# Performance work log

Hardware: AMD Instinct MI355X
Metric: run time of the kernel (lower is better)

The kernel has to match this reference:

```python
import jax, jax.numpy as jnp
import numpy as np

B, E, H, V, D2, T = 128, 512, 512, 32000, 1024, 17

def setup_inputs() -> dict:
    key = jax.random.key(0)
    ks = jax.random.split(key, 13)
    s = 0.02
    return {
        "features": jax.random.normal(ks[0], (B, 512), dtype=jnp.float32),
        "captions": jax.random.randint(ks[1], (B, T), 0, V, dtype=jnp.int32),
        "W_enc": jax.random.normal(ks[2], (512, E), dtype=jnp.float32) * s,
        "b_enc": jnp.zeros((E,), dtype=jnp.float32),
        "emb": jax.random.normal(ks[3], (V, E), dtype=jnp.float32) * s,
        "W_ih": jax.random.normal(ks[4], (4 * H, E), dtype=jnp.float32) * s,
        "b_ih": jnp.zeros((4 * H,), dtype=jnp.float32),
        "W_hh": jax.random.normal(ks[5], (4 * H, H), dtype=jnp.float32) * s,
        "b_hh": jnp.zeros((4 * H,), dtype=jnp.float32),
        "W_d2": jax.random.normal(ks[6], (H, D2), dtype=jnp.float32) * s,
        "b_d2": jnp.zeros((D2,), dtype=jnp.float32),
        "W_last": jax.random.normal(ks[7], (D2, V), dtype=jnp.float32) * s,
        "b_last": jnp.zeros((V,), dtype=jnp.float32),
    }


def reference(features, captions, W_enc, b_enc, emb, W_ih, b_ih, W_hh, b_hh, W_d2, b_d2, W_last, b_last):
    # encoder_last: project frozen-resnet features [B,512] -> [B,E]
    feat = features @ W_enc + b_enc
    # embed captions[:, :-1] -> [B,16,E], prepend image feature -> [B,17,E]
    e = emb[captions[:, :-1]]
    x = jnp.concatenate([feat[:, None, :], e], axis=1)  # [B,T,E]

    def step(carry, xt):
        h, c = carry
        gates = xt @ W_ih.T + b_ih + h @ W_hh.T + b_hh  # [B,4H]
        i, f, g, o = jnp.split(gates, 4, axis=-1)  # PyTorch LSTMCell gate order
        i, f, o = jax.nn.sigmoid(i), jax.nn.sigmoid(f), jax.nn.sigmoid(o)
        g = jnp.tanh(g)
        c = f * c + i * g
        h = o * jnp.tanh(c)
        return (h, c), h

    h0 = jnp.zeros((x.shape[0], H), dtype=x.dtype)
    c0 = jnp.zeros((x.shape[0], H), dtype=x.dtype)
    _, hs = jax.lax.scan(step, (h0, c0), jnp.swapaxes(x, 0, 1))  # [T,B,H]
    hs = jnp.swapaxes(hs, 0, 1)  # [B,T,H]

    out = jax.nn.relu(hs @ W_d2 + b_d2)       # [B,T,D2]
    logits = out @ W_last + b_last            # [B,T,V]
    return jax.nn.softmax(logits, axis=2)
```

## Files before the change

### kernel.cpp

```cpp
#include <hip/hip_runtime.h>
#include <hip/hip_bf16.h>

#define B_   128
#define T_   17
#define E_   512
#define H_   512
#define V_   32000
#define D2_  1024
#define MR_  (B_*T_)

typedef __attribute__((ext_vector_type(8))) short short8;
typedef __attribute__((ext_vector_type(4))) float f32x4;

__device__ __forceinline__ unsigned short f2b(float f) {
  unsigned u = __float_as_uint(f);
  u += 0x7FFFu + ((u >> 16) & 1u);
  return (unsigned short)(u >> 16);
}
__device__ __forceinline__ float sigf(float x) { return 1.f / (1.f + __expf(-x)); }
__device__ __forceinline__ float tanhfast(float x) {
  x = fminf(fmaxf(x, -15.f), 15.f);
  float e = __expf(2.f * x);
  return (e - 1.f) / (e + 1.f);
}

__device__ __forceinline__ void async16(const void* g, void* l) {
  __builtin_amdgcn_global_load_lds((const __attribute__((address_space(1))) unsigned int*)g,
                                   (__attribute__((address_space(3))) unsigned int*)l,
                                   16, 0, 0);
}

template<int EPI, int SWZ>
__global__ __launch_bounds__(256, 2)
void gemm_bt(const unsigned short* __restrict__ A,
             const unsigned short* __restrict__ Bt,
             void* __restrict__ C,
             const float* __restrict__ bias0,
             const float* __restrict__ bias1,
             int N, int K, int nbm, int nwork)
{
  __shared__ unsigned short sA[128 * 32];
  __shared__ unsigned short sB[128 * 32];

  int f = blockIdx.x;
  if constexpr (SWZ) {
    int per = (nwork + 7) >> 3;
    f = (f & 7) * per + (f >> 3);
    if (f >= nwork) return;
  }
  const size_t bm = (size_t)(f % nbm) * 128;
  const size_t bn = (size_t)(f / nbm) * 128;

  const int tid  = threadIdx.x;
  const int lane = tid & 63;
  const int wave = tid >> 6;
  const int wm   = wave & 1;
  const int wn   = wave >> 1;

  const int sRow   = wave * 32 + (lane >> 2);
  const int gchunk = (lane & 3) ^ ((sRow >> 2) & 3);

  const unsigned short* gA  = A  + (bm + sRow)      * (size_t)K + gchunk * 8;
  const unsigned short* gA2 = A  + (bm + sRow + 16) * (size_t)K + gchunk * 8;
  const unsigned short* gB  = Bt + (bn + sRow)      * (size_t)K + gchunk * 8;
  const unsigned short* gB2 = Bt + (bn + sRow + 16) * (size_t)K + gchunk * 8;

  unsigned short* lA  = &sA[wave * 1024];
  unsigned short* lA2 = &sA[wave * 1024 + 512];
  unsigned short* lB  = &sB[wave * 1024];
  unsigned short* lB2 = &sB[wave * 1024 + 512];

  f32x4 acc[4][4] = {};
  const int fm = lane & 15;
  const int q  = lane >> 4;

  for (int kt = 0; kt < K; kt += 32) {
    async16(gA  + kt, lA);
    async16(gA2 + kt, lA2);
    async16(gB  + kt, lB);
    async16(gB2 + kt, lB2);
    __syncthreads();

    short8 af[4], bfv[4];
#pragma unroll
    for (int i = 0; i < 4; i++) {
      int ra = wm * 64 + i * 16 + fm;
      af[i]  = *(const short8*)&sA[ra * 32 + ((q ^ ((ra >> 2) & 3)) * 8)];
      int rb = wn * 64 + i * 16 + fm;
      bfv[i] = *(const short8*)&sB[rb * 32 + ((q ^ ((rb >> 2) & 3)) * 8)];
    }
#pragma unroll
    for (int i = 0; i < 4; i++)
#pragma unroll
      for (int j = 0; j < 4; j++)
        acc[i][j] = __builtin_amdgcn_mfma_f32_16x16x32_bf16(af[i], bfv[j], acc[i][j], 0, 0, 0);
    __syncthreads();
  }

#pragma unroll
  for (int i = 0; i < 4; i++) {
#pragma unroll
    for (int j = 0; j < 4; j++) {
      size_t col = bn + wn * 64 + j * 16 + fm;
      float bv = 0.f;
      if constexpr (EPI == 0) {
        size_t oc = ((col & 3) << 9) + (col >> 2);
        bv = bias0[oc] + bias1[oc];
      }
      if constexpr (EPI == 2 || EPI == 3 || EPI == 4) bv = bias0[col];
#pragma unroll
      for (int r = 0; r < 4; r++) {
        size_t row = bm + wm * 64 + i * 16 + q * 4 + r;
        float v = acc[i][j][r] + bv;
        if constexpr (EPI == 2) {
          v = v > 0.f ? v : 0.f;
          ((unsigned short*)C)[row * N + col] = f2b(v);
        } else if constexpr (EPI == 3) {
          ((unsigned short*)C)[row * N + col] = f2b(v);
        } else {
          ((float*)C)[row * N + col] = v;
        }
      }
    }
  }
}

#define STG(gp, lb, row0, kt) do { \
    async16((gp) + (size_t)(row0) * K + (kt),       (lb) + (row0) * 64); \
    async16((gp) + (size_t)((row0) + 8) * K + (kt), (lb) + ((row0) + 8) * 64); \
  } while (0)

template<int EPI>
__global__ __launch_bounds__(512, 2)
void gemm256(const unsigned short* __restrict__ A,
             const unsigned short* __restrict__ Bt,
             void* __restrict__ C,
             const float* __restrict__ bias0,
             int N, int K, int M, int nbm, int nwork)
{
  __shared__ unsigned short sA[2][256 * 64];
  __shared__ unsigned short sB[2][256 * 64];

  int f = blockIdx.x;
  const int per = (nwork + 7) >> 3;
  f = (f & 7) * per + (f >> 3);
  if (f >= nwork) return;
  int bmx = (f % nbm) * 256;
  if (bmx > M - 256) bmx = M - 256;
  const size_t bm = (size_t)bmx;
  const size_t bn = (size_t)(f / nbm) * 256;

  const int tid  = threadIdx.x;
  const int lane = tid & 63;
  const int wave = tid >> 6;
  const int wm   = wave >> 2;
  const int wn   = wave & 3;
  const int fm   = lane & 15;
  const int q    = lane >> 4;

  const int cs = (((lane & 7) ^ (lane >> 3)) << 3);
  const unsigned short* gA = A  + (bm + (lane >> 3)) * (size_t)K + cs;
  const unsigned short* gB = Bt + (bn + (lane >> 3)) * (size_t)K + cs;

  const int NT = K >> 6;
  const int arow0 = (wave & 3) * 16 + (wave >> 2) * 128;
  const int arow1 = arow0 + 64;
  const int brow0 = wave * 16;
  const int brow1 = brow0 + 128;

  STG(gB, sB[0], brow0, 0);
  STG(gB, sB[0], brow1, 0);
  STG(gA, sA[0], arow0, 0);
  STG(gA, sA[0], arow1, 0);
  if (NT > 1) {
    STG(gB, sB[1], brow0, 64);
    STG(gB, sB[1], brow1, 64);
    STG(gA, sA[1], arow0, 64);
    asm volatile("s_waitcnt vmcnt(6)" ::: "memory");
  } else {
    asm volatile("s_waitcnt vmcnt(0)" ::: "memory");
  }
  __builtin_amdgcn_s_barrier();

  f32x4 acc[8][4] = {};
  short8 breg[4][2];

  for (int t = 0; t < NT; ++t) {
    const int bi = t & 1;
    const unsigned short* sa = sA[bi];
    const unsigned short* sb = sB[bi];
    const int kt1 = (t + 1) << 6;
    const int kt2 = (t + 2) << 6;
    const bool st1 = (t + 1) < NT;
    const bool st2 = (t + 2) < NT;

#pragma unroll
    for (int mq = 0; mq < 4; ++mq) {
      short8 a[2][2];
#pragma unroll
      for (int ff = 0; ff < 2; ff++) {
        const int r = wm * 128 + (2 * mq + ff) * 16 + fm;
#pragma unroll
        for (int ks = 0; ks < 2; ks++)
          a[ff][ks] = *(const short8*)&sa[r * 64 + (((ks * 4 + q) ^ (r & 7)) << 3)];
      }
      if (mq == 0) {
#pragma unroll
        for (int j = 0; j < 4; j++) {
          const int r = wn * 64 + j * 16 + fm;
#pragma unroll
          for (int ks = 0; ks < 2; ks++)
            breg[j][ks] = *(const short8*)&sb[r * 64 + (((ks * 4 + q) ^ (r & 7)) << 3)];
        }
        if (st1) STG(gA, sA[bi ^ 1], arow1, kt1);
      } else if (mq == 1) {
        if (st2) STG(gB, sB[bi], brow0, kt2);
      } else if (mq == 2) {
        if (st2) STG(gB, sB[bi], brow1, kt2);
      } else {
        if (st2) STG(gA, sA[bi], arow0, kt2);
      }

      asm volatile("" ::: "memory");
      __builtin_amdgcn_s_barrier();
      asm volatile("s_waitcnt lgkmcnt(0)" ::: "memory");
      __builtin_amdgcn_sched_barrier(0);
      __builtin_amdgcn_s_setprio(1);
#pragma unroll
      for (int ff = 0; ff < 2; ff++)
#pragma unroll
        for (int j = 0; j < 4; j++)
#pragma unroll
          for (int ks = 0; ks < 2; ks++)
            acc[2 * mq + ff][j] =
              __builtin_amdgcn_mfma_f32_16x16x32_bf16(a[ff][ks], breg[j][ks],
                                                      acc[2 * mq + ff][j], 0, 0, 0);
      __builtin_amdgcn_s_setprio(0);
      __builtin_amdgcn_sched_barrier(0);
      if (mq == 3) {
        if (st2)      asm volatile("s_waitcnt vmcnt(6)" ::: "memory");
        else if (st1) asm volatile("s_waitcnt vmcnt(0)" ::: "memory");
      }
      asm volatile("" ::: "memory");
      __builtin_amdgcn_s_barrier();
    }
  }

#pragma unroll
  for (int i = 0; i < 8; i++) {
#pragma unroll
    for (int j = 0; j < 4; j++) {
      const size_t col = bn + wn * 64 + j * 16 + fm;
      const float bv = bias0[col];
#pragma unroll
      for (int r = 0; r < 4; r++) {
        const size_t row = bm + wm * 128 + i * 16 + q * 4 + r;
        const float v = acc[i][j][r] + bv;
        if constexpr (EPI == 3) ((unsigned short*)C)[row * (size_t)N + col] = f2b(v);
        else                    ((float*)C)[row * (size_t)N + col] = v;
      }
    }
  }
}
#undef STG

__global__ __launch_bounds__(256)
void lstm_step(const unsigned short* __restrict__ hprev,
               const unsigned short* __restrict__ Whh,
               const float* __restrict__ Gt,
               float* __restrict__ c,
               unsigned short* __restrict__ hout,
               unsigned short* __restrict__ hsb,
               int t)
{
  __shared__ char smem[131072];
  unsigned short* sA = (unsigned short*)smem;
  unsigned short* sB = (unsigned short*)(smem + 65536);
  float* gl = (float*)smem;

  const int tid  = threadIdx.x;
  const int lane = tid & 63;
  const int wave = tid >> 6;
  const int wm   = wave & 1;
  const int wn   = wave >> 1;
  const int n0   = blockIdx.x * 128;

  const int lr = lane >> 5;
  const int lp = lane & 31;

  f32x4 acc[4][4] = {};
  const int fm = lane & 15;
  const int q  = lane >> 4;

  for (int kt = 0; kt < 512; kt += 256) {
#pragma unroll
    for (int s = 0; s < 16; s++) {
      int row = wave * 32 + s * 2 + lr;
      int gch = lp ^ (row & 7);
      async16(hprev + (size_t)row * 512 + kt + gch * 8,
              sA + wave * 8192 + s * 512 + lane * 8);
      async16(Whh + (size_t)(n0 + row) * 512 + kt + gch * 8,
              sB + wave * 8192 + s * 512 + lane * 8);
    }
    __syncthreads();

#pragma unroll
    for (int kk = 0; kk < 8; kk++) {
      int ch = kk * 4 + q;
      short8 af[4], bfv[4];
#pragma unroll
      for (int i = 0; i < 4; i++) {
        int ra = wm * 64 + i * 16 + fm;
        af[i]  = *(const short8*)&sA[ra * 256 + ((ch ^ (ra & 7)) * 8)];
        int rb = wn * 64 + i * 16 + fm;
        bfv[i] = *(const short8*)&sB[rb * 256 + ((ch ^ (rb & 7)) * 8)];
      }
#pragma unroll
      for (int i = 0; i < 4; i++)
#pragma unroll
        for (int j = 0; j < 4; j++)
          acc[i][j] = __builtin_amdgcn_mfma_f32_16x16x32_bf16(af[i], bfv[j], acc[i][j], 0, 0, 0);
    }
    __syncthreads();
  }

#pragma unroll
  for (int i = 0; i < 4; i++)
#pragma unroll
    for (int j = 0; j < 4; j++)
#pragma unroll
      for (int r = 0; r < 4; r++)
        gl[(wm * 64 + i * 16 + q * 4 + r) * 132 + wn * 64 + j * 16 + fm] = acc[i][j][r];
  __syncthreads();

#pragma unroll
  for (int it = 0; it < 16; it++) {
    int p   = it * 256 + tid;
    int row = p >> 5;
    int ul  = p & 31;
    float4 a4 = *(float4*)&gl[row * 132 + ul * 4];
    float4 G4 = *(const float4*)&Gt[row * 2048 + n0 + ul * 4];
    float gi = a4.x + G4.x, gf = a4.y + G4.y, gg = a4.z + G4.z, go = a4.w + G4.w;
    int gu  = (n0 >> 2) + ul;
    int idx = row * 512 + gu;
    float cn = sigf(gf) * c[idx] + sigf(gi) * tanhfast(gg);
    c[idx] = cn;
    float hn = sigf(go) * tanhfast(cn);
    unsigned short h16 = f2b(hn);
    hout[idx] = h16;
    hsb[((size_t)row * T_ + t) * 512 + gu] = h16;
  }
}

__global__ void lstm_point0(const float* __restrict__ G0, float* __restrict__ c,
                            unsigned short* __restrict__ hb, unsigned short* __restrict__ hsb) {
  int idx = blockIdx.x * 256 + threadIdx.x;
  int b = idx >> 9, u = idx & 511;
  float4 g4 = ((const float4*)(G0 + (size_t)b * 2048))[u];
  float cn = sigf(g4.x) * tanhfast(g4.z);
  c[idx] = cn;
  float hn = sigf(g4.w) * tanhfast(cn);
  unsigned short h16 = f2b(hn);
  hb[idx] = h16;
  hsb[((size_t)b * T_ + 0) * 512 + u] = h16;
}

__global__ void permute_cvt2(const float* __restrict__ Wih, const float* __restrict__ Whh,
                             unsigned short* __restrict__ dih, unsigned short* __restrict__ dhh) {
  int p = blockIdx.x;
  const float* src = (p < 2048) ? Wih : Whh;
  unsigned short* dst = (p < 2048) ? dih : dhh;
  int pp = p & 2047;
  int ir = ((pp & 3) << 9) + (pp >> 2);
  float4 v = ((const float4*)(src + (size_t)ir * 512))[threadIdx.x];
  ushort4 o;
  o.x = f2b(v.x); o.y = f2b(v.y); o.z = f2b(v.z); o.w = f2b(v.w);
  ((ushort4*)(dst + (size_t)p * 512))[threadIdx.x] = o;
}

__global__ void transpose_cvt(const float* __restrict__ src, unsigned short* __restrict__ dst,
                              int K, int N) {
  __shared__ float tile[32][33];
  int n0 = blockIdx.x * 32, k0 = blockIdx.y * 32;
  int tcol = threadIdx.x & 31, trow = threadIdx.x >> 5;
  for (int r = trow; r < 32; r += 8)
    tile[r][tcol] = src[(size_t)(k0 + r) * N + n0 + tcol];
  __syncthreads();
  for (int r = trow; r < 32; r += 8)
    dst[(size_t)(n0 + r) * K + k0 + tcol] = f2b(tile[tcol][r]);
}

__global__ __launch_bounds__(256) void encode(const float* __restrict__ features,
                                              const float* __restrict__ W_enc,
                                              const float* __restrict__ b_enc,
                                              unsigned short* __restrict__ xb) {
  __shared__ float fs[512];
  int b = blockIdx.y, e = blockIdx.x * 256 + threadIdx.x;
  fs[threadIdx.x]       = features[b * 512 + threadIdx.x];
  fs[threadIdx.x + 256] = features[b * 512 + threadIdx.x + 256];
  __syncthreads();
  float acc = 0.f;
#pragma unroll 8
  for (int k = 0; k < 512; k++) acc += fs[k] * W_enc[(size_t)k * 512 + e];
  xb[(size_t)b * 512 + e] = f2b(acc + b_enc[e]);
}

__global__ void embed_k(const int* __restrict__ captions, const float* __restrict__ emb,
                        unsigned short* __restrict__ xb) {
  int t = blockIdx.x + 1, b = blockIdx.y;
  int tok = captions[b * T_ + (t - 1)];
  float4 v = ((const float4*)(emb + (size_t)tok * 512))[threadIdx.x];
  ushort4 o;
  o.x = f2b(v.x); o.y = f2b(v.y); o.z = f2b(v.z); o.w = f2b(v.w);
  ((ushort4*)(xb + (size_t)(t * B_ + b) * 512))[threadIdx.x] = o;
}

__global__ __launch_bounds__(1024) void softmax_b(const unsigned short* __restrict__ lg,
                                                  float* __restrict__ out) {
  __shared__ float ps[1024];
  const uint4* r4 = (const uint4*)(lg + (size_t)blockIdx.x * V_);
  float* orow = out + (size_t)blockIdx.x * V_;
  int tid = threadIdx.x;
  float v[4][8];
  float s = 0.f;
#pragma unroll
  for (int u = 0; u < 4; u++) {
    int i = u * 1024 + tid;
    if (i < 4000) {
      uint4 w = r4[i];
      unsigned a[4] = {w.x, w.y, w.z, w.w};
#pragma unroll
      for (int k = 0; k < 4; k++) {
        float lo = __uint_as_float(a[k] << 16);
        float hi = __uint_as_float(a[k] & 0xffff0000u);
        float e0 = __expf(lo), e1 = __expf(hi);
        v[u][2 * k] = e0; v[u][2 * k + 1] = e1;
        s += e0 + e1;
      }
    }
  }
  ps[tid] = s;
  __syncthreads();
  for (int o = 512; o > 0; o >>= 1) {
    if (tid < o) ps[tid] += ps[tid + o];
    __syncthreads();
  }
  float inv = 1.f / ps[0];
#pragma unroll
  for (int u = 0; u < 4; u++) {
    int i = u * 1024 + tid;
    if (i < 4000) {
      float4 o1 = {v[u][0] * inv, v[u][1] * inv, v[u][2] * inv, v[u][3] * inv};
      float4 o2 = {v[u][4] * inv, v[u][5] * inv, v[u][6] * inv, v[u][7] * inv};
      ((float4*)(orow + (size_t)i * 8))[0] = o1;
      ((float4*)(orow + (size_t)i * 8))[1] = o2;
    }
  }
}

__global__ __launch_bounds__(1024) void softmax_f(float* __restrict__ out) {
  __shared__ float ps[1024];
  float* r = out + (size_t)blockIdx.x * V_;
  int tid = threadIdx.x;
  float v[32];
  float s = 0.f;
#pragma unroll
  for (int u = 0; u < 32; u++) {
    int i = u * 1024 + tid;
    if (i < V_) { float e = __expf(r[i]); v[u] = e; s += e; }
  }
  ps[tid] = s;
  __syncthreads();
  for (int o = 512; o > 0; o >>= 1) {
    if (tid < o) ps[tid] += ps[tid + o];
    __syncthreads();
  }
  float inv = 1.f / ps[0];
#pragma unroll
  for (int u = 0; u < 32; u++) {
    int i = u * 1024 + tid;
    if (i < V_) r[i] = v[u] * inv;
  }
}

extern "C" void kernel_launch(void* const* d_in, const int* in_sizes, int n_in,
                              void* d_out, int out_size, void* d_ws, size_t ws_size,
                              hipStream_t stream) {
  const float* features = (const float*)d_in[0];
  const int*   captions = (const int*)d_in[1];
  const float* W_enc  = (const float*)d_in[2];
  const float* b_enc  = (const float*)d_in[3];
  const float* emb    = (const float*)d_in[4];
  const float* W_ih   = (const float*)d_in[5];
  const float* b_ih   = (const float*)d_in[6];
  const float* W_hh   = (const float*)d_in[7];
  const float* b_hh   = (const float*)d_in[8];
  const float* W_d2   = (const float*)d_in[9];
  const float* b_d2   = (const float*)d_in[10];
  const float* W_last = (const float*)d_in[11];
  const float* b_last = (const float*)d_in[12];
  float* out = (float*)d_out;

  char* ws = (char*)d_ws;
  size_t off = 0;
  auto alloc = [&](size_t bytes) -> void* {
    void* p = ws + off;
    off += (bytes + 255) & ~(size_t)255;
    return p;
  };
  unsigned short* xb     = (unsigned short*)alloc((size_t)MR_ * E_ * 2);
  unsigned short* Wb_ih  = (unsigned short*)alloc((size_t)4 * H_ * E_ * 2);
  unsigned short* Wb_hh  = (unsigned short*)alloc((size_t)4 * H_ * H_ * 2);
  unsigned short* Wb_d2t = (unsigned short*)alloc((size_t)D2_ * H_ * 2);
  unsigned short* Wb_lt  = (unsigned short*)alloc((size_t)V_ * D2_ * 2);
  float*          G      = (float*)alloc((size_t)MR_ * 4 * H_ * 4);
  float*          cst    = (float*)alloc((size_t)B_ * H_ * 4);
  unsigned short* hb0    = (unsigned short*)alloc((size_t)B_ * H_ * 2);
  unsigned short* hb1    = (unsigned short*)alloc((size_t)B_ * H_ * 2);
  unsigned short* hsb    = (unsigned short*)alloc((size_t)MR_ * H_ * 2);
  unsigned short* outb   = (unsigned short*)alloc((size_t)MR_ * D2_ * 2);
  unsigned short* lgb    = (unsigned short*)alloc((size_t)MR_ * V_ * 2);
  const bool bf16_logits = (off <= ws_size);
  (void)in_sizes; (void)n_in; (void)out_size;

  permute_cvt2<<<4096, 128, 0, stream>>>(W_ih, W_hh, Wb_ih, Wb_hh);
  transpose_cvt<<<dim3(D2_ / 32, H_ / 32), 256, 0, stream>>>(W_d2, Wb_d2t, H_, D2_);

  encode<<<dim3(2, B_), 256, 0, stream>>>(features, W_enc, b_enc, xb);
  embed_k<<<dim3(T_ - 1, B_), 128, 0, stream>>>(captions, emb, xb);

  gemm_bt<0, 0><<<17 * 16, 256, 0, stream>>>(xb, Wb_ih, G, b_ih, b_hh, 4 * H_, E_, 17, 17 * 16);

  lstm_point0<<<B_ * H_ / 256, 256, 0, stream>>>(G, cst, hb0, hsb);
  for (int t = 1; t < T_; t++) {
    unsigned short* hp = (t & 1) ? hb0 : hb1;
    unsigned short* hc = (t & 1) ? hb1 : hb0;
    lstm_step<<<16, 256, 0, stream>>>(hp, Wb_hh, G + (size_t)t * B_ * 4 * H_, cst, hc, hsb, t);
  }

  transpose_cvt<<<dim3(V_ / 32, D2_ / 32), 256, 0, stream>>>(W_last, Wb_lt, D2_, V_);

  gemm_bt<2, 0><<<17 * 8, 256, 0, stream>>>(hsb, Wb_d2t, outb, b_d2, nullptr, D2_, H_, 17, 17 * 8);

  const int nbm2   = 9;
  const int nwork2 = nbm2 * (V_ / 256);
  const int per2   = (nwork2 + 7) / 8;
  if (bf16_logits) {
    gemm256<3><<<8 * per2, 512, 0, stream>>>(outb, Wb_lt, lgb, b_last, V_, D2_, MR_, nbm2, nwork2);
    softmax_b<<<MR_, 1024, 0, stream>>>(lgb, out);
  } else {
    gemm256<4><<<8 * per2, 512, 0, stream>>>(outb, Wb_lt, out, b_last, V_, D2_, MR_, nbm2, nwork2);
    softmax_f<<<MR_, 1024, 0, stream>>>(out);
  }
}
```

Baseline: 943.6 us.

## Software-pipeline LDS fragment loads against MFMA in the 256x256 GEMM

Restructures the gemm256 main loop so A and B fragments for the next phase are read from shared memory while the current phase's MFMAs execute. It uses double-buffered register fragments (af0/af1, bregA/bregB) and unrolls the loop by two tiles. This removes the per-phase barrier and lgkmcnt stall that sat between the LDS reads and the matrix ops. In exchange it raises register pressure, and it assumes NT is even, since the loop unrolls by two without a remainder tile.

After: 962.7 us. 1.02x slower.

```diff
diff --git a/kernel.cpp b/kernel.cpp
--- a/kernel.cpp
+++ b/kernel.cpp
@@ -130,6 +130,75 @@
     async16((gp) + (size_t)((row0) + 8) * K + (kt), (lb) + ((row0) + 8) * 64); \
   } while (0)
 
+#define LDA(dst, sa_, mq_) do { \
+    _Pragma("unroll") \
+    for (int ff = 0; ff < 2; ff++) { \
+      const int r_ = wm * 128 + ((mq_) * 2 + ff) * 16 + fm; \
+      _Pragma("unroll") \
+      for (int ks = 0; ks < 2; ks++) \
+        dst[ff][ks] = *(const short8*)&(sa_)[r_ * 64 + (((ks * 4 + q) ^ (r_ & 7)) << 3)]; \
+    } } while (0)
+
+#define LDB(dst, sb_) do { \
+    _Pragma("unroll") \
+    for (int j = 0; j < 4; j++) { \
+      const int r_ = wn * 64 + j * 16 + fm; \
+      _Pragma("unroll") \
+      for (int ks = 0; ks < 2; ks++) \
+        dst[j][ks] = *(const short8*)&(sb_)[r_ * 64 + (((ks * 4 + q) ^ (r_ & 7)) << 3)]; \
+    } } while (0)
+
+#define MMA(ab, bb, mq_) do { \
+    _Pragma("unroll") \
+    for (int ff = 0; ff < 2; ff++) \
+      _Pragma("unroll") \
+      for (int j = 0; j < 4; j++) \
+        _Pragma("unroll") \
+        for (int ks = 0; ks < 2; ks++) \
+          acc[(mq_) * 2 + ff][j] = __builtin_amdgcn_mfma_f32_16x16x32_bf16( \
+              ab[ff][ks], bb[j][ks], acc[(mq_) * 2 + ff][j], 0, 0, 0); \
+  } while (0)
+
+#define PH_TAIL() do { \
+    asm volatile("s_waitcnt lgkmcnt(0)" ::: "memory"); \
+    __builtin_amdgcn_sched_barrier(0); \
+    __builtin_amdgcn_s_barrier(); \
+  } while (0)
+
+#define TILE(BI, BC, BN, T) do { \
+    const int t_ = (T); \
+    const int kt1 = (t_ + 1) << 6, kt2 = (t_ + 2) << 6; \
+    const bool st1 = (t_ + 1) < NT, st2 = (t_ + 2) < NT; \
+     \
+    LDA(af1, sA[BI], 1); \
+    if (st1) STG(gA, sA[(BI) ^ 1], arow1, kt1); \
+    __builtin_amdgcn_sched_barrier(0); \
+    __builtin_amdgcn_s_setprio(1); MMA(af0, BC, 0); __builtin_amdgcn_s_setprio(0); \
+    PH_TAIL(); \
+     \
+    LDA(af0, sA[BI], 2); \
+    if (st2) STG(gB, sB[BI], brow0, kt2); \
+    __builtin_amdgcn_sched_barrier(0); \
+    __builtin_amdgcn_s_setprio(1); MMA(af1, BC, 1); __builtin_amdgcn_s_setprio(0); \
+    PH_TAIL(); \
+     \
+    LDA(af1, sA[BI], 3); \
+    if (st2) STG(gB, sB[BI], brow1, kt2); \
+    __builtin_amdgcn_sched_barrier(0); \
+    __builtin_amdgcn_s_setprio(1); MMA(af0, BC, 2); __builtin_amdgcn_s_setprio(0); \
+    asm volatile("s_waitcnt lgkmcnt(0)" ::: "memory"); \
+    if (st2) { asm volatile("s_waitcnt vmcnt(4)" ::: "memory"); } \
+    else     { asm volatile("s_waitcnt vmcnt(0)" ::: "memory"); } \
+    __builtin_amdgcn_sched_barrier(0); \
+    __builtin_amdgcn_s_barrier(); \
+     \
+    if (st1) { LDA(af0, sA[(BI) ^ 1], 0); LDB(BN, sB[(BI) ^ 1]); } \
+    if (st2) STG(gA, sA[BI], arow0, kt2); \
+    __builtin_amdgcn_sched_barrier(0); \
+    __builtin_amdgcn_s_setprio(1); MMA(af1, BC, 3); __builtin_amdgcn_s_setprio(0); \
+    PH_TAIL(); \
+  } while (0)
+
 template<int EPI>
 __global__ __launch_bounds__(512, 2)
 void gemm256(const unsigned short* __restrict__ A,
@@ -183,67 +252,17 @@
   __builtin_amdgcn_s_barrier();
 
   f32x4 acc[8][4] = {};
-  short8 breg[4][2];
-
-  for (int t = 0; t < NT; ++t) {
-    const int bi = t & 1;
-    const unsigned short* sa = sA[bi];
-    const unsigned short* sb = sB[bi];
-    const int kt1 = (t + 1) << 6;
-    const int kt2 = (t + 2) << 6;
-    const bool st1 = (t + 1) < NT;
-    const bool st2 = (t + 2) < NT;
-
-#pragma unroll
-    for (int mq = 0; mq < 4; ++mq) {
-      short8 a[2][2];
-#pragma unroll
-      for (int ff = 0; ff < 2; ff++) {
-        const int r = wm * 128 + (2 * mq + ff) * 16 + fm;
-#pragma unroll
-        for (int ks = 0; ks < 2; ks++)
-          a[ff][ks] = *(const short8*)&sa[r * 64 + (((ks * 4 + q) ^ (r & 7)) << 3)];
-      }
-      if (mq == 0) {
-#pragma unroll
-        for (int j = 0; j < 4; j++) {
-          const int r = wn * 64 + j * 16 + fm;
-#pragma unroll
-          for (int ks = 0; ks < 2; ks++)
-            breg[j][ks] = *(const short8*)&sb[r * 64 + (((ks * 4 + q) ^ (r & 7)) << 3)];
-        }
-        if (st1) STG(gA, sA[bi ^ 1], arow1, kt1);
-      } else if (mq == 1) {
-        if (st2) STG(gB, sB[bi], brow0, kt2);
-      } else if (mq == 2) {
-        if (st2) STG(gB, sB[bi], brow1, kt2);
-      } else {
-        if (st2) STG(gA, sA[bi], arow0, kt2);
-      }
-
-      asm volatile("" ::: "memory");
-      __builtin_amdgcn_s_barrier();
-      asm volatile("s_waitcnt lgkmcnt(0)" ::: "memory");
-      __builtin_amdgcn_sched_barrier(0);
-      __builtin_amdgcn_s_setprio(1);
-#pragma unroll
-      for (int ff = 0; ff < 2; ff++)
-#pragma unroll
-        for (int j = 0; j < 4; j++)
-#pragma unroll
-          for (int ks = 0; ks < 2; ks++)
-            acc[2 * mq + ff][j] =
-              __builtin_amdgcn_mfma_f32_16x16x32_bf16(a[ff][ks], breg[j][ks],
-                                                      acc[2 * mq + ff][j], 0, 0, 0);
-      __builtin_amdgcn_s_setprio(0);
-      __builtin_amdgcn_sched_barrier(0);
-      if (mq == 3) {
-        if (st2)      asm volatile("s_waitcnt vmcnt(6)" ::: "memory");
-        else if (st1) asm volatile("s_waitcnt vmcnt(0)" ::: "memory");
-      }
-      asm volatile("" ::: "memory");
-      __builtin_amdgcn_s_barrier();
-    }
+  short8 af0[2][2], af1[2][2];
+  short8 bregA[4][2], bregB[4][2];
+
+  LDA(af0, sA[0], 0);
+  LDB(bregA, sB[0]);
+  asm volatile("s_waitcnt lgkmcnt(0)" ::: "memory");
+  __builtin_amdgcn_sched_barrier(0);
+
+  for (int tt = 0; tt < NT; tt += 2) {
+    TILE(0, bregA, bregB, tt);
+    TILE(1, bregB, bregA, tt + 1);
   }
 
 #pragma unroll
@@ -262,6 +281,11 @@
     }
   }
 }
+#undef TILE
+#undef PH_TAIL
+#undef MMA
+#undef LDB
+#undef LDA
 #undef STG
 
 __global__ __launch_bounds__(256)
```
